# Kernel optimization log

Hardware: AMD Instinct MI355X
Metric: run time of the kernel (lower is better)

## Reference

```python
import jax, jax.numpy as jnp
import numpy as np

N, D, H, K = 50000, 384, 128, 16
WALK_STEPS = 3
EPS = 1e-8


def setup_inputs() -> dict:
    key = jax.random.key(0)
    ks = jax.random.split(key, 7)
    emb = jax.random.normal(ks[0], (N, D), dtype=jnp.float32)
    qv = jax.random.normal(ks[1], (D,), dtype=jnp.float32)
    W1 = jax.random.normal(ks[2], (2 * D, H), dtype=jnp.float32) * (1.0 / np.sqrt(2 * D))
    b1 = jax.random.normal(ks[3], (H,), dtype=jnp.float32) * 0.01
    W2 = jax.random.normal(ks[4], (H, K), dtype=jnp.float32) * (1.0 / np.sqrt(H))
    b2 = jax.random.normal(ks[5], (K,), dtype=jnp.float32) * 0.01
    nbr = jax.random.randint(ks[6], (N, K), 0, N, dtype=jnp.int64)
    return {"emb": emb, "qv": qv, "W1": W1, "b1": b1, "W2": W2, "b2": b2, "nbr": nbr}


def reference(emb, qv, W1, b1, W2, b2, nbr):
    n, k = nbr.shape
    # Per-node coin: coin_net(concat(emb_i, qv)) -> normalized rank-1 outer product.
    # (Coin does not depend on the walk state, so compute once; original recomputes
    # the identical values every step.)
    inp = jnp.concatenate([emb, jnp.broadcast_to(qv, (n, qv.shape[0]))], axis=-1)  # [n, 2d]
    h = jax.nn.relu(inp @ W1 + b1)                                                 # [n, H]
    amps = h @ W2 + b2                                                             # [n, k]
    amps = amps / (jnp.linalg.norm(amps, axis=-1, keepdims=True) + EPS)
    coin = amps[:, :, None] * amps[:, None, :]                                     # [n, k, k]
    fro = jnp.linalg.norm(coin.reshape(n, -1), axis=-1)[:, None, None]
    coin = coin / (fro + EPS)
    # Reverse-slot lookup: for edge slot (i, idx) with j = nbr[i, idx], find first p
    # with nbr[j, p] == i (the .index(i) in the original); missing -> dropped.
    match = nbr[nbr] == jnp.arange(n, dtype=nbr.dtype)[:, None, None]              # [n, k, k]
    rev_idx = jnp.argmax(match, axis=-1)                                           # [n, k]
    rev_mask = jnp.any(match, axis=-1)                                             # [n, k]
    flat_tgt = (nbr * k + rev_idx).reshape(-1)
    # Initial state is real and the coin is real (cast to cfloat in the original),
    # so the walk state stays real-valued; |z|^2 == z^2 here.
    state = jnp.full((n, k), 1.0 / np.sqrt(n * k), dtype=emb.dtype)

    def step(state, _):
        s_p = jnp.einsum('nij,nj->ni', coin, state)                                # coin @ state
        contrib = jnp.where(rev_mask, s_p, 0.0)
        new = jnp.zeros(n * k, dtype=state.dtype).at[flat_tgt].add(contrib.reshape(-1))
        new = new.reshape(n, k)
        new = new / (jnp.sqrt(jnp.sum(new * new)) + EPS)
        return new, None

    state, _ = jax.lax.scan(step, state, None, length=WALK_STEPS)
    probs = jnp.sum(state * state, axis=1)
    return jnp.nan_to_num(probs, nan=0.0, posinf=1.0, neginf=0.0)
```

## Files before the change

kernel.cpp:

```cpp
#include <hip/hip_runtime.h>
#include <math.h>

#define N_NODES 50000
#define DIM     384
#define HID     128
#define KN      16
#define NK      (N_NODES * KN)
#define EPSF    1e-8f

#define NSLAB   1563
#define SLABCAP 8
#define CAPR2   1024
#define BT2     1024

#define OFF_CNT   1024u
#define OFF_SLABE 8192u
#define OFF_SLABT 58368u
#define OFF_AS    108544u
#define OFF_FA    158720u
#define OFF_SM    208896u

__global__ __launch_bounds__(512)
void scan_coin_kernel(const int* __restrict__ nbr, const float* __restrict__ emb,
                      const float* __restrict__ qv, const float* __restrict__ W1,
                      const float* __restrict__ b1, const float* __restrict__ W2,
                      const float* __restrict__ b2,
                      int* __restrict__ cnt, int* __restrict__ slab_e,
                      int* __restrict__ slab_t, float* __restrict__ as_g,
                      float* __restrict__ fa_g, float* __restrict__ sm_g,
                      float* __restrict__ out) {
    __shared__ int   wcnt[8];
    __shared__ int   recE[SLABCAP];
    __shared__ int   recT[SLABCAP];
    __shared__ float sq[DIM];
    __shared__ float prt[4 * HID];
    __shared__ float c1s[HID];
    __shared__ float sh[HID];
    __shared__ float prt2[32 * KN];
    __shared__ float samps[KN];

    int b = blockIdx.x, tid = threadIdx.x;
    int e = b * 512 + tid;
    if (e < N_NODES) out[e] = 0.f;

    bool valid = (e < NK);
    int ecl = valid ? e : 0;
    int j = nbr[ecl];
    const int4* rp = (const int4*)(nbr + (size_t)j * KN);
    int4 r0 = rp[0], r1 = rp[1], r2 = rp[2], r3 = rp[3];
    int i = ecl >> 4;
    unsigned m = 0;
    m |= (unsigned)(r0.x == i) << 0;  m |= (unsigned)(r0.y == i) << 1;
    m |= (unsigned)(r0.z == i) << 2;  m |= (unsigned)(r0.w == i) << 3;
    m |= (unsigned)(r1.x == i) << 4;  m |= (unsigned)(r1.y == i) << 5;
    m |= (unsigned)(r1.z == i) << 6;  m |= (unsigned)(r1.w == i) << 7;
    m |= (unsigned)(r2.x == i) << 8;  m |= (unsigned)(r2.y == i) << 9;
    m |= (unsigned)(r2.z == i) << 10; m |= (unsigned)(r2.w == i) << 11;
    m |= (unsigned)(r3.x == i) << 12; m |= (unsigned)(r3.y == i) << 13;
    m |= (unsigned)(r3.z == i) << 14; m |= (unsigned)(r3.w == i) << 15;
    bool flag = valid && (m != 0);
    int p = __ffs(m) - 1;

    unsigned long long bal = __ballot(flag);
    int lane = tid & 63, w = tid >> 6;
    if (lane == 0) wcnt[w] = __popcll(bal);
    __syncthreads();
    int wb = 0, tot = 0;
    #pragma unroll
    for (int x = 0; x < 8; ++x) { int v = wcnt[x]; tot += v; if (x < w) wb += v; }
    int tot_ = (tot > SLABCAP) ? SLABCAP : tot;
    if (tid == 0) cnt[b] = tot_;
    if (flag) {
        int rank = wb + __popcll(bal & ((1ull << lane) - 1ull));
        if (rank < SLABCAP) { recE[rank] = e; recT[rank] = j * KN + p; }
    }
    if (tot_ == 0) return;
    __syncthreads();
    if (tid < tot_) {
        slab_e[b * SLABCAP + tid] = recE[tid];
        slab_t[b * SLABCAP + tid] = recT[tid];
    }

    if (tid < DIM) sq[tid] = qv[tid];
    __syncthreads();
    int c = tid & 127, g = tid >> 7;
    {
        const float* wp = W1 + (size_t)(DIM + g * 96) * HID + c;
        float acc = 0.f;
        #pragma unroll 16
        for (int d = 0; d < 96; ++d)
            acc += sq[g * 96 + d] * wp[(size_t)d * HID];
        prt[g * HID + c] = acc;
    }
    __syncthreads();
    if (tid < HID)
        c1s[tid] = b1[tid] + prt[tid] + prt[HID + tid] + prt[2 * HID + tid] + prt[3 * HID + tid];

    for (int q = 0; q < tot_; ++q) {
        int e2 = recE[q];
        int node = e2 >> 4;
        __syncthreads();
        if (tid < DIM) sq[tid] = emb[(size_t)node * DIM + tid];
        __syncthreads();
        const float* wp = W1 + (size_t)(g * 96) * HID + c;
        float acc = 0.f;
        #pragma unroll 16
        for (int d = 0; d < 96; ++d)
            acc += sq[g * 96 + d] * wp[(size_t)d * HID];
        prt[g * HID + c] = acc;
        __syncthreads();
        if (tid < HID)
            sh[tid] = fmaxf(c1s[tid] + prt[tid] + prt[HID + tid]
                            + prt[2 * HID + tid] + prt[3 * HID + tid], 0.f);
        __syncthreads();
        int k = tid & 15, g2 = tid >> 4;
        float a2 = 0.f;
        #pragma unroll
        for (int jj = 0; jj < 4; ++jj)
            a2 += sh[g2 * 4 + jj] * W2[(size_t)(g2 * 4 + jj) * KN + k];
        prt2[g2 * KN + k] = a2;
        __syncthreads();
        if (tid < KN) {
            float s = b2[tid];
            #pragma unroll
            for (int g3 = 0; g3 < 32; ++g3) s += prt2[g3 * KN + tid];
            samps[tid] = s;
        }
        __syncthreads();
        if (tid == 0) {
            float ss = 0.f;
            #pragma unroll
            for (int t2 = 0; t2 < KN; ++t2) ss += samps[t2] * samps[t2];
            float inv_na = 1.f / (sqrtf(ss) + EPSF);
            float fro = 0.f, sa = 0.f;
            #pragma unroll
            for (int t2 = 0; t2 < KN; ++t2) {
                float av = samps[t2] * inv_na;
                fro += av * av; sa += av;
            }
            float av_src = samps[e2 & 15] * inv_na;
            float invf = 1.f / (fro + EPSF);
            as_g[b * SLABCAP + q] = av_src;
            fa_g[b * SLABCAP + q] = av_src * invf;
            sm_g[b * SLABCAP + q] = sa;
        }
    }
}

__global__ __launch_bounds__(BT2)
void walk_kernel(const int* __restrict__ cnt, const int* __restrict__ slab_e,
                 const int* __restrict__ slab_t, const float* __restrict__ as_g,
                 const float* __restrict__ fa_g, const float* __restrict__ sm_g,
                 float* __restrict__ out) {
    __shared__ int   baseL[2048];
    __shared__ int   cntL[2048];
    __shared__ int   erL[CAPR2];
    __shared__ int   nodeL[CAPR2];
    __shared__ int   trecL[CAPR2];
    __shared__ int   segLo[CAPR2];
    __shared__ int   segHi[CAPR2];
    __shared__ float asL[CAPR2];
    __shared__ float faL[CAPR2];
    __shared__ float d0L[CAPR2];
    __shared__ float stA[CAPR2];
    __shared__ float stB[CAPR2];
    __shared__ float dtL[CAPR2];
    __shared__ int   wsumL[16];
    __shared__ float redL[16];

    int tid = threadIdx.x;
    int lane = tid & 63, w = tid >> 6;

    int s0 = tid * 2, s1 = tid * 2 + 1;
    int lc0 = (s0 < NSLAB) ? cnt[s0] : 0;
    int lc1 = (s1 < NSLAB) ? cnt[s1] : 0;
    int ts = lc0 + lc1;
    int vinc = ts;
    #pragma unroll
    for (int off = 1; off < 64; off <<= 1) {
        int n = __shfl_up(vinc, off, 64);
        if (lane >= off) vinc += n;
    }
    if (lane == 63) wsumL[w] = vinc;
    __syncthreads();
    int wb = 0, Mtot = 0;
    #pragma unroll
    for (int x = 0; x < 16; ++x) { int v = wsumL[x]; Mtot += v; if (x < w) wb += v; }
    int base = wb + vinc - ts;
    baseL[s0] = base;       cntL[s0] = lc0;
    baseL[s1] = base + lc0; cntL[s1] = lc1;
    int M = (Mtot > CAPR2) ? CAPR2 : Mtot;
    const float S0 = 1.0f / sqrtf((float)N_NODES * (float)KN);

    for (int q = 0; q < lc0; ++q) {
        int r = base + q;
        if (r < CAPR2) {
            int e = slab_e[s0 * SLABCAP + q];
            erL[r] = e; nodeL[r] = e >> 4;
            trecL[r] = slab_t[s0 * SLABCAP + q];
            asL[r] = as_g[s0 * SLABCAP + q];
            faL[r] = fa_g[s0 * SLABCAP + q];
            d0L[r] = S0 * sm_g[s0 * SLABCAP + q];
            stA[r] = 0.f; stB[r] = 0.f;
        }
    }
    for (int q = 0; q < lc1; ++q) {
        int r = base + lc0 + q;
        if (r < CAPR2) {
            int e = slab_e[s1 * SLABCAP + q];
            erL[r] = e; nodeL[r] = e >> 4;
            trecL[r] = slab_t[s1 * SLABCAP + q];
            asL[r] = as_g[s1 * SLABCAP + q];
            faL[r] = fa_g[s1 * SLABCAP + q];
            d0L[r] = S0 * sm_g[s1 * SLABCAP + q];
            stA[r] = 0.f; stB[r] = 0.f;
        }
    }
    __syncthreads();

    for (int r = tid; r < M; r += BT2) {
        int t  = trecL[r];
        int bt = t >> 9;
        int bs = baseL[bt], bc = cntL[bt];
        int tr = -1;
        for (int q = 0; q < bc; ++q) {
            int r2 = bs + q;
            if (r2 < CAPR2 && erL[r2] == t) { tr = r2; break; }
        }
        trecL[r] = tr;
        int nd = nodeL[r];
        int lo = r; while (lo > 0 && nodeL[lo - 1] == nd) --lo;
        int hi = r; while (hi < M - 1 && nodeL[hi + 1] == nd) ++hi;
        segLo[r] = lo; segHi[r] = hi;
    }
    __syncthreads();

    auto NORM = [&](float* buf, float* zb) {
        float part = 0.f;
        for (int r = tid; r < M; r += BT2) part += buf[r] * buf[r];
        #pragma unroll
        for (int off = 32; off > 0; off >>= 1) part += __shfl_xor(part, off, 64);
        if (lane == 0) redL[w] = part;
        __syncthreads();
        float tot = 0.f;
        #pragma unroll
        for (int x = 0; x < 16; ++x) tot += redL[x];
        float si = 1.0f / (sqrtf(tot) + EPSF);
        for (int r = tid; r < M; r += BT2) {
            buf[r] *= si;
            if (zb) zb[r] = 0.f;
        }
        __syncthreads();
    };
    auto DOT = [&](const float* st) {
        for (int r = tid; r < M; r += BT2) {
            float d = 0.f;
            int hi = segHi[r];
            for (int r2 = segLo[r]; r2 <= hi; ++r2) d += asL[r2] * st[r2];
            dtL[r] = d;
        }
        __syncthreads();
    };

    for (int r = tid; r < M; r += BT2)
        if (trecL[r] >= 0) atomicAdd(&stA[trecL[r]], faL[r] * d0L[r]);
    __syncthreads();
    NORM(stA, d0L);

    DOT(stA);
    for (int r = tid; r < M; r += BT2)
        if (trecL[r] >= 0) atomicAdd(&stB[trecL[r]], faL[r] * dtL[r]);
    __syncthreads();
    NORM(stB, nullptr);

    DOT(stB);
    for (int r = tid; r < M; r += BT2)
        if (trecL[r] >= 0) atomicAdd(&d0L[trecL[r]], faL[r] * dtL[r]);
    __syncthreads();
    NORM(d0L, nullptr);

    for (int r = tid; r < M; r += BT2) {
        float v = d0L[r];
        atomicAdd(&out[nodeL[r]], v * v);
    }
}

extern "C" void kernel_launch(void* const* d_in, const int* in_sizes, int n_in,
                              void* d_out, int out_size, void* d_ws, size_t ws_size,
                              hipStream_t stream) {
    const float* emb = (const float*)d_in[0];
    const float* qv  = (const float*)d_in[1];
    const float* W1  = (const float*)d_in[2];
    const float* b1  = (const float*)d_in[3];
    const float* W2  = (const float*)d_in[4];
    const float* b2  = (const float*)d_in[5];
    const int*   nbr = (const int*)d_in[6];
    float*       out = (float*)d_out;

    char* ws = (char*)d_ws;
    int*   cnt     = (int*)(ws + OFF_CNT);
    int*   slab_e  = (int*)(ws + OFF_SLABE);
    int*   slab_t  = (int*)(ws + OFF_SLABT);
    float* as_g    = (float*)(ws + OFF_AS);
    float* fa_g    = (float*)(ws + OFF_FA);
    float* sm_g    = (float*)(ws + OFF_SM);

    scan_coin_kernel<<<NSLAB, 512, 0, stream>>>(
        nbr, emb, qv, W1, b1, W2, b2, cnt, slab_e, slab_t,
        as_g, fa_g, sm_g, out);
    walk_kernel<<<1, BT2, 0, stream>>>(
        cnt, slab_e, slab_t, as_g, fa_g, sm_g, out);
}
```

Before: 31.69 us.

## Pack slab records into int2/float4 and shrink walk kernel to 256 threads

Per-edge records in the workspace are packed into one int2 (edge, target) and one float4 (amplitude, scaled amplitude, sum), replacing five separate arrays, so each record is fetched with fewer, wider loads. The single-block walk kernel drops from 1024 to 256 threads, with each thread scanning 7 slab counts instead of 2, which makes the block-wide reductions and barriers cheaper. The cost is more serial work per thread in the prefix scan and record gather, plus fewer threads sharing the per-record loops.

```diff
diff --git a/kernel.cpp b/kernel.cpp
--- a/kernel.cpp
+++ b/kernel.cpp
@@ -11,23 +11,20 @@
 #define NSLAB   1563
 #define SLABCAP 8
 #define CAPR2   1024
-#define BT2     1024
+#define BT2     256
+#define SPT     7
 
 #define OFF_CNT   1024u
-#define OFF_SLABE 8192u
-#define OFF_SLABT 58368u
-#define OFF_AS    108544u
-#define OFF_FA    158720u
-#define OFF_SM    208896u
+#define OFF_ET    8192u
+#define OFF_R4    108544u
 
 __global__ __launch_bounds__(512)
 void scan_coin_kernel(const int* __restrict__ nbr, const float* __restrict__ emb,
                       const float* __restrict__ qv, const float* __restrict__ W1,
                       const float* __restrict__ b1, const float* __restrict__ W2,
                       const float* __restrict__ b2,
-                      int* __restrict__ cnt, int* __restrict__ slab_e,
-                      int* __restrict__ slab_t, float* __restrict__ as_g,
-                      float* __restrict__ fa_g, float* __restrict__ sm_g,
+                      int* __restrict__ cnt, int2* __restrict__ slab_et,
+                      float4* __restrict__ rec4,
                       float* __restrict__ out) {
     __shared__ int   wcnt[8];
     __shared__ int   recE[SLABCAP];
@@ -76,10 +73,8 @@
     }
     if (tot_ == 0) return;
     __syncthreads();
-    if (tid < tot_) {
-        slab_e[b * SLABCAP + tid] = recE[tid];
-        slab_t[b * SLABCAP + tid] = recT[tid];
-    }
+    if (tid < tot_)
+        slab_et[b * SLABCAP + tid] = make_int2(recE[tid], recT[tid]);
 
     if (tid < DIM) sq[tid] = qv[tid];
     __syncthreads();
@@ -140,20 +135,16 @@
             }
             float av_src = samps[e2 & 15] * inv_na;
             float invf = 1.f / (fro + EPSF);
-            as_g[b * SLABCAP + q] = av_src;
-            fa_g[b * SLABCAP + q] = av_src * invf;
-            sm_g[b * SLABCAP + q] = sa;
+            rec4[b * SLABCAP + q] = make_float4(av_src, av_src * invf, sa, 0.f);
         }
     }
 }
 
 __global__ __launch_bounds__(BT2)
-void walk_kernel(const int* __restrict__ cnt, const int* __restrict__ slab_e,
-                 const int* __restrict__ slab_t, const float* __restrict__ as_g,
-                 const float* __restrict__ fa_g, const float* __restrict__ sm_g,
-                 float* __restrict__ out) {
-    __shared__ int   baseL[2048];
-    __shared__ int   cntL[2048];
+void walk_kernel(const int* __restrict__ cnt, const int2* __restrict__ slab_et,
+                 const float4* __restrict__ rec4, float* __restrict__ out) {
+    __shared__ int   baseL[256 * SPT];
+    __shared__ int   cntL[256 * SPT];
     __shared__ int   erL[CAPR2];
     __shared__ int   nodeL[CAPR2];
     __shared__ int   trecL[CAPR2];
@@ -165,16 +156,20 @@
     __shared__ float stA[CAPR2];
     __shared__ float stB[CAPR2];
     __shared__ float dtL[CAPR2];
-    __shared__ int   wsumL[16];
-    __shared__ float redL[16];
+    __shared__ int   wsumL[4];
+    __shared__ float redL[4];
 
     int tid = threadIdx.x;
     int lane = tid & 63, w = tid >> 6;
 
-    int s0 = tid * 2, s1 = tid * 2 + 1;
-    int lc0 = (s0 < NSLAB) ? cnt[s0] : 0;
-    int lc1 = (s1 < NSLAB) ? cnt[s1] : 0;
-    int ts = lc0 + lc1;
+    int s0 = tid * SPT;
+    int lc[SPT]; int ts = 0;
+    #pragma unroll
+    for (int k = 0; k < SPT; ++k) {
+        int s = s0 + k;
+        int v = (s < NSLAB) ? cnt[s] : 0;
+        lc[k] = v; ts += v;
+    }
     int vinc = ts;
     #pragma unroll
     for (int off = 1; off < 64; off <<= 1) {
@@ -185,36 +180,28 @@
     __syncthreads();
     int wb = 0, Mtot = 0;
     #pragma unroll
-    for (int x = 0; x < 16; ++x) { int v = wsumL[x]; Mtot += v; if (x < w) wb += v; }
-    int base = wb + vinc - ts;
-    baseL[s0] = base;       cntL[s0] = lc0;
-    baseL[s1] = base + lc0; cntL[s1] = lc1;
+    for (int x = 0; x < 4; ++x) { int v = wsumL[x]; Mtot += v; if (x < w) wb += v; }
+    int run = wb + vinc - ts;
     int M = (Mtot > CAPR2) ? CAPR2 : Mtot;
     const float S0 = 1.0f / sqrtf((float)N_NODES * (float)KN);
 
-    for (int q = 0; q < lc0; ++q) {
-        int r = base + q;
-        if (r < CAPR2) {
-            int e = slab_e[s0 * SLABCAP + q];
-            erL[r] = e; nodeL[r] = e >> 4;
-            trecL[r] = slab_t[s0 * SLABCAP + q];
-            asL[r] = as_g[s0 * SLABCAP + q];
-            faL[r] = fa_g[s0 * SLABCAP + q];
-            d0L[r] = S0 * sm_g[s0 * SLABCAP + q];
-            stA[r] = 0.f; stB[r] = 0.f;
-        }
-    }
-    for (int q = 0; q < lc1; ++q) {
-        int r = base + lc0 + q;
-        if (r < CAPR2) {
-            int e = slab_e[s1 * SLABCAP + q];
-            erL[r] = e; nodeL[r] = e >> 4;
-            trecL[r] = slab_t[s1 * SLABCAP + q];
-            asL[r] = as_g[s1 * SLABCAP + q];
-            faL[r] = fa_g[s1 * SLABCAP + q];
-            d0L[r] = S0 * sm_g[s1 * SLABCAP + q];
-            stA[r] = 0.f; stB[r] = 0.f;
-        }
+    #pragma unroll
+    for (int k = 0; k < SPT; ++k) {
+        int s = s0 + k;
+        if (s < NSLAB) { baseL[s] = run; cntL[s] = lc[k]; }
+        for (int q = 0; q < lc[k]; ++q) {
+            int r = run + q;
+            if (r < CAPR2) {
+                int2   et = slab_et[s * SLABCAP + q];
+                float4 rc = rec4[s * SLABCAP + q];
+                erL[r] = et.x; nodeL[r] = et.x >> 4;
+                trecL[r] = et.y;
+                asL[r] = rc.x; faL[r] = rc.y;
+                d0L[r] = S0 * rc.z;
+                stA[r] = 0.f; stB[r] = 0.f;
+            }
+        }
+        run += lc[k];
     }
     __syncthreads();
 
@@ -242,9 +229,7 @@
         for (int off = 32; off > 0; off >>= 1) part += __shfl_xor(part, off, 64);
         if (lane == 0) redL[w] = part;
         __syncthreads();
-        float tot = 0.f;
-        #pragma unroll
-        for (int x = 0; x < 16; ++x) tot += redL[x];
+        float tot = redL[0] + redL[1] + redL[2] + redL[3];
         float si = 1.0f / (sqrtf(tot) + EPSF);
         for (int r = tid; r < M; r += BT2) {
             buf[r] *= si;
@@ -298,16 +283,11 @@
     float*       out = (float*)d_out;
 
     char* ws = (char*)d_ws;
-    int*   cnt     = (int*)(ws + OFF_CNT);
-    int*   slab_e  = (int*)(ws + OFF_SLABE);
-    int*   slab_t  = (int*)(ws + OFF_SLABT);
-    float* as_g    = (float*)(ws + OFF_AS);
-    float* fa_g    = (float*)(ws + OFF_FA);
-    float* sm_g    = (float*)(ws + OFF_SM);
+    int*    cnt     = (int*)(ws + OFF_CNT);
+    int2*   slab_et = (int2*)(ws + OFF_ET);
+    float4* rec4    = (float4*)(ws + OFF_R4);
 
     scan_coin_kernel<<<NSLAB, 512, 0, stream>>>(
-        nbr, emb, qv, W1, b1, W2, b2, cnt, slab_e, slab_t,
-        as_g, fa_g, sm_g, out);
-    walk_kernel<<<1, BT2, 0, stream>>>(
-        cnt, slab_e, slab_t, as_g, fa_g, sm_g, out);
+        nbr, emb, qv, W1, b1, W2, b2, cnt, slab_et, rec4, out);
+    walk_kernel<<<1, BT2, 0, stream>>>(cnt, slab_et, rec4, out);
 }
```

Result: slower. 34.24 us (+8.0%).
